# Kernel optimization log

Hardware: AMD Instinct MI355X
Metric: run time of the kernel (lower is better)

The kernel has to match this reference:

```python
import jax, jax.numpy as jnp
import numpy as np

B, N, S = 32, 4096, 11          # batch, n_inputs (64x64 feature map), n_slots
D_IN, D, MLP = 512, 512, 2048   # input feat dim, qkv_size, mlp hidden
ITERS = 3                       # num_iterations
EPS_ATTN = 1e-8                 # renormalize epsilon
EPS_LN = 1e-5                   # torch LayerNorm default eps


def layer_norm(x, g, b, eps=EPS_LN):
    mu = jnp.mean(x, axis=-1, keepdims=True)
    var = jnp.mean(jnp.square(x - mu), axis=-1, keepdims=True)
    return (x - mu) * jax.lax.rsqrt(var + eps) * g + b


def setup_inputs() -> dict:
    key = jax.random.key(0)
    ks = jax.random.split(key, 16)
    s = 0.02
    return {
        "slots": jax.random.normal(ks[0], (B, S, D), jnp.float32),
        "inputs": jax.random.normal(ks[1], (B, N, D_IN), jnp.float32),
        # input LayerNorm
        "ln_in_g": jnp.ones((D_IN,), jnp.float32),
        "ln_in_b": jnp.zeros((D_IN,), jnp.float32),
        # k / v projections (with bias, like nn.Linear)
        "Wk": jax.random.normal(ks[2], (D_IN, D), jnp.float32) * s,
        "bk": jnp.zeros((D,), jnp.float32),
        "Wv": jax.random.normal(ks[3], (D_IN, D), jnp.float32) * s,
        "bv": jnp.zeros((D,), jnp.float32),
        # query LayerNorm + bias-free q projection
        "ln_q_g": jnp.ones((D,), jnp.float32),
        "ln_q_b": jnp.zeros((D,), jnp.float32),
        "Wq": jax.random.normal(ks[4], (D, D), jnp.float32) * s,
        # GRUCell: gate order (r, z, n), torch layout [3D, D]
        "W_ih": jax.random.normal(ks[5], (3 * D, D), jnp.float32) * s,
        "b_ih": jnp.zeros((3 * D,), jnp.float32),
        "W_hh": jax.random.normal(ks[6], (3 * D, D), jnp.float32) * s,
        "b_hh": jnp.zeros((3 * D,), jnp.float32),
        # MLP: LN -> Linear -> ReLU -> Linear (no residual in source)
        "ln_m_g": jnp.ones((D,), jnp.float32),
        "ln_m_b": jnp.zeros((D,), jnp.float32),
        "W1": jax.random.normal(ks[7], (D, MLP), jnp.float32) * s,
        "b1": jnp.zeros((MLP,), jnp.float32),
        "W2": jax.random.normal(ks[8], (MLP, D), jnp.float32) * s,
        "b2": jnp.zeros((D,), jnp.float32),
    }


def reference(slots, inputs, ln_in_g, ln_in_b, Wk, bk, Wv, bv,
              ln_q_g, ln_q_b, Wq, W_ih, b_ih, W_hh, b_hh,
              ln_m_g, ln_m_b, W1, b1, W2, b2):
    # inputs LN + k/v projections (computed once, outside the loop)
    x = layer_norm(inputs, ln_in_g, ln_in_b)          # [B, N, D_IN]
    k = x @ Wk + bk                                   # [B, N, D]
    v = x @ Wv + bv                                   # [B, N, D]
    scale = 1.0 / jnp.sqrt(jnp.asarray(D, slots.dtype))

    for _ in range(ITERS):
        # q projection
        q = layer_norm(slots, ln_q_g, ln_q_b) @ Wq    # [B, S, D]
        # inverted attention: softmax over slot (query) axis
        logits = jnp.einsum('bsd,bnd->bsn', q * scale, k)  # [B, S, N]
        attn = jax.nn.softmax(logits, axis=-2)        # over S (inverted)
        # renormalize over keys (mean norm)
        attn = attn / (jnp.sum(attn, axis=-1, keepdims=True) + EPS_ATTN)
        updates = jnp.einsum('bsn,bnd->bsd', attn, v)  # [B, S, D]

        # GRUCell(updates, slots) -- torch semantics, gate order (r, z, n)
        gi = updates @ W_ih.T + b_ih                  # [B, S, 3D]
        gh = slots @ W_hh.T + b_hh                    # [B, S, 3D]
        ir, iz, in_ = jnp.split(gi, 3, axis=-1)
        hr, hz, hn = jnp.split(gh, 3, axis=-1)
        r = jax.nn.sigmoid(ir + hr)
        z = jax.nn.sigmoid(iz + hz)
        n = jnp.tanh(in_ + r * hn)
        slots = (1.0 - z) * n + z * slots

        # MLP (note: source assigns slots = mlp(slots), no residual)
        h = layer_norm(slots, ln_m_g, ln_m_b)
        slots = jax.nn.relu(h @ W1 + b1) @ W2 + b2
    return slots
```

## Files before the change

kernel.cpp:

```cpp
#include <hip/hip_runtime.h>
#include <cstdint>
#include <cstddef>

typedef short bf16x8 __attribute__((ext_vector_type(8)));
typedef float floatx4 __attribute__((ext_vector_type(4)));
typedef unsigned short ushort4v __attribute__((ext_vector_type(4)));

#define LN_EPS 1e-5f
#define ATTN_EPS 1e-8f
#define NCHUNK 16

__device__ __forceinline__ unsigned short f2bf(float f) {
    unsigned int u = __float_as_uint(f);
    u += 0x7fffu + ((u >> 16) & 1u);
    return (unsigned short)(u >> 16);
}

__device__ __forceinline__ void load_lds16(const void* gp, void* lp) {
    __builtin_amdgcn_global_load_lds(
        (__attribute__((address_space(1))) void*)gp,
        (__attribute__((address_space(3))) void*)lp,
        16, 0, 0);
}

template<bool OUT_BF16, bool QDOT>
__global__ __launch_bounds__(256) void ln512_kernel(
        const float* __restrict__ x, const float* __restrict__ g, const float* __restrict__ b,
        void* __restrict__ out, int total_rows, int data_rows, float outscale,
        const float* __restrict__ wqbk, float* __restrict__ cbuf) {
    int row = blockIdx.x * 4 + (threadIdx.x >> 6);
    int lane = threadIdx.x & 63;
    if (row >= total_rows) return;
    int rr = row < data_rows ? row : data_rows - 1;
    const float4* xr = (const float4*)(x + (size_t)rr * 512);
    float4 a0 = xr[lane];
    float4 a1 = xr[lane + 64];
    float s  = a0.x + a0.y + a0.z + a0.w + a1.x + a1.y + a1.z + a1.w;
    float ss = a0.x*a0.x + a0.y*a0.y + a0.z*a0.z + a0.w*a0.w
             + a1.x*a1.x + a1.y*a1.y + a1.z*a1.z + a1.w*a1.w;
    #pragma unroll
    for (int off = 32; off > 0; off >>= 1) {
        s  += __shfl_xor(s, off, 64);
        ss += __shfl_xor(ss, off, 64);
    }
    float mu = s * (1.0f / 512.0f);
    float var = ss * (1.0f / 512.0f) - mu * mu;
    float rstd = rsqrtf(var + LN_EPS);
    float4 g0 = ((const float4*)g)[lane];
    float4 g1 = ((const float4*)g)[lane + 64];
    float4 b0 = ((const float4*)b)[lane];
    float4 b1 = ((const float4*)b)[lane + 64];
    float y[8];
    y[0] = ((a0.x - mu) * rstd * g0.x + b0.x) * outscale;
    y[1] = ((a0.y - mu) * rstd * g0.y + b0.y) * outscale;
    y[2] = ((a0.z - mu) * rstd * g0.z + b0.z) * outscale;
    y[3] = ((a0.w - mu) * rstd * g0.w + b0.w) * outscale;
    y[4] = ((a1.x - mu) * rstd * g1.x + b1.x) * outscale;
    y[5] = ((a1.y - mu) * rstd * g1.y + b1.y) * outscale;
    y[6] = ((a1.z - mu) * rstd * g1.z + b1.z) * outscale;
    y[7] = ((a1.w - mu) * rstd * g1.w + b1.w) * outscale;
    if (QDOT) {
        float4 w0 = ((const float4*)wqbk)[lane];
        float4 w1 = ((const float4*)wqbk)[lane + 64];
        float cd = y[0]*w0.x + y[1]*w0.y + y[2]*w0.z + y[3]*w0.w
                 + y[4]*w1.x + y[5]*w1.y + y[6]*w1.z + y[7]*w1.w;
        #pragma unroll
        for (int off = 32; off > 0; off >>= 1) cd += __shfl_xor(cd, off, 64);
        if (lane == 0) cbuf[row] = cd;
    }
    if (OUT_BF16) {
        unsigned short* orow = (unsigned short*)out + (size_t)row * 512;
        ushort4v o0, o1;
        o0.x = f2bf(y[0]); o0.y = f2bf(y[1]); o0.z = f2bf(y[2]); o0.w = f2bf(y[3]);
        o1.x = f2bf(y[4]); o1.y = f2bf(y[5]); o1.z = f2bf(y[6]); o1.w = f2bf(y[7]);
        *(ushort4v*)(orow + lane * 4) = o0;
        *(ushort4v*)(orow + 256 + lane * 4) = o1;
    } else {
        float* orow = (float*)out + (size_t)row * 512;
        *(float4*)(orow + lane * 4) = make_float4(y[0], y[1], y[2], y[3]);
        *(float4*)(orow + 256 + lane * 4) = make_float4(y[4], y[5], y[6], y[7]);
    }
}

__device__ __forceinline__ void tr32(const float* __restrict__ in, unsigned short* __restrict__ out,
                                     int R, int C, int bx, int by, float (*tile)[33]) {
    int tx = threadIdx.x & 31, ty = threadIdx.x >> 5;
    #pragma unroll
    for (int i = 0; i < 32; i += 8)
        tile[ty + i][tx] = in[(size_t)(by + ty + i) * C + bx + tx];
    __syncthreads();
    #pragma unroll
    for (int i = 0; i < 32; i += 8)
        out[(size_t)(bx + ty + i) * R + by + tx] = f2bf(tile[tx][ty + i]);
}

__device__ __forceinline__ void rowdot512(const float* __restrict__ in, const float* __restrict__ vec,
                                          float* __restrict__ out, int row) {
    int lane = threadIdx.x & 63;
    const float4* r0 = (const float4*)(in + (size_t)row * 512);
    float4 a0 = r0[lane], a1 = r0[lane + 64];
    float4 v0 = ((const float4*)vec)[lane], v1 = ((const float4*)vec)[lane + 64];
    float d = a0.x*v0.x + a0.y*v0.y + a0.z*v0.z + a0.w*v0.w
            + a1.x*v1.x + a1.y*v1.y + a1.z*v1.z + a1.w*v1.w;
    #pragma unroll
    for (int off = 32; off > 0; off >>= 1) d += __shfl_xor(d, off, 64);
    if (lane == 0) out[row] = d;
}

__global__ __launch_bounds__(256) void prep_all(
        const float* __restrict__ Wk, const float* __restrict__ Wq,
        const float* __restrict__ Wv, const float* __restrict__ W_ih,
        const float* __restrict__ W_hh, const float* __restrict__ W1,
        const float* __restrict__ W2, const float* __restrict__ slots_in,
        const float* __restrict__ bk, const float* __restrict__ bv,
        unsigned short* __restrict__ Wk_b, unsigned short* __restrict__ Wq_b,
        unsigned short* __restrict__ Wv_b, unsigned short* __restrict__ Wih_b,
        unsigned short* __restrict__ Whh_b, unsigned short* __restrict__ W1T,
        unsigned short* __restrict__ W2T, unsigned short* __restrict__ slbf,
        float* __restrict__ wqbk, float* __restrict__ bvW) {
    __shared__ float tile[32][33];
    const int b = blockIdx.x;
    const int t = threadIdx.x;
    if (b < 1024) {
        int idx = b * 256 + t; Wk_b[idx] = f2bf(Wk[idx]);
    } else if (b < 2048) {
        int idx = (b - 1024) * 256 + t; Wq_b[idx] = f2bf(Wq[idx]);
    } else if (b < 3072) {
        int idx = (b - 2048) * 256 + t; Wv_b[idx] = f2bf(Wv[idx]);
    } else if (b < 6144) {
        int idx = (b - 3072) * 256 + t; Wih_b[idx] = f2bf(W_ih[idx]);
    } else if (b < 9216) {
        int idx = (b - 6144) * 256 + t; Whh_b[idx] = f2bf(W_hh[idx]);
    } else if (b < 10240) {
        int i = b - 9216;
        tr32(W1, W1T, 512, 2048, (i & 63) * 32, (i >> 6) * 32, tile);
    } else if (b < 11264) {
        int i = b - 10240;
        tr32(W2, W2T, 2048, 512, (i & 15) * 32, (i >> 4) * 32, tile);
    } else if (b < 12032) {
        int idx = (b - 11264) * 256 + t;
        int row = idx >> 9, d = idx & 511;
        int rr = row < 352 ? row : 351;
        slbf[idx] = f2bf(slots_in[(size_t)rr * 512 + d]);
    } else if (b < 12160) {
        int row = (b - 12032) * 4 + (t >> 6);
        rowdot512(Wq, bk, wqbk, row);
    } else {
        int row = (b - 12160) * 4 + (t >> 6);
        rowdot512(W_ih, bv, bvW, row);
    }
}

template<int BMODE, bool RELU, int OUT_MODE>
__device__ __forceinline__ void hgemm_core(
        const unsigned short* __restrict__ A, const unsigned short* __restrict__ Bt,
        const float* __restrict__ bias, const float* __restrict__ bvW,
        const float* __restrict__ coef, float* __restrict__ Cf,
        unsigned short* __restrict__ Cb, int m0, int n0, int N, int K,
        unsigned short* As, unsigned short* Bs) {
    const int t = threadIdx.x;
    const int lane = t & 63;
    const int w = t >> 6;
    const int wm = w >> 1, wn = w & 1;
    const int quad = lane >> 4;
    const int l15 = lane & 15;
    floatx4 acc[2][2];
    #pragma unroll
    for (int i = 0; i < 2; ++i)
        #pragma unroll
        for (int j = 0; j < 2; ++j)
            #pragma unroll
            for (int r = 0; r < 4; ++r) acc[i][j][r] = 0.0f;

    for (int k0 = 0; k0 < K; k0 += 64) {
        #pragma unroll
        for (int p = 0; p < 2; ++p) {
            const int s = p * 256 + t;
            const int row = s >> 3;
            const int c = (s & 7) ^ (row & 7);
            const int ldsoff = (s - lane) * 16;
            load_lds16(A  + (size_t)(m0 + row) * K + k0 + c * 8, (char*)As + ldsoff);
            load_lds16(Bt + (size_t)(n0 + row) * K + k0 + c * 8, (char*)Bs + ldsoff);
        }
        __builtin_amdgcn_s_waitcnt(0);
        __syncthreads();
        #pragma unroll
        for (int h = 0; h < 2; ++h) {
            bf16x8 af[2], bfr[2];
            #pragma unroll
            for (int i = 0; i < 2; ++i) {
                const int row = wm * 32 + i * 16 + l15;
                const int cp = ((h << 2) | quad) ^ (l15 & 7);
                af[i] = *(const bf16x8*)(As + row * 64 + cp * 8);
            }
            #pragma unroll
            for (int j = 0; j < 2; ++j) {
                const int row = wn * 32 + j * 16 + l15;
                const int cp = ((h << 2) | quad) ^ (l15 & 7);
                bfr[j] = *(const bf16x8*)(Bs + row * 64 + cp * 8);
            }
            #pragma unroll
            for (int i = 0; i < 2; ++i)
                #pragma unroll
                for (int j = 0; j < 2; ++j)
                    acc[i][j] = __builtin_amdgcn_mfma_f32_16x16x32_bf16(af[i], bfr[j], acc[i][j], 0, 0, 0);
        }
        __syncthreads();
    }
    #pragma unroll
    for (int j = 0; j < 2; ++j) {
        const int n = n0 + wn * 32 + j * 16 + l15;
        const float bb = (BMODE >= 1) ? bias[n] : 0.0f;
        const float bw = (BMODE == 2) ? bvW[n] : 0.0f;
        #pragma unroll
        for (int i = 0; i < 2; ++i) {
            #pragma unroll
            for (int r = 0; r < 4; ++r) {
                const int m = m0 + wm * 32 + i * 16 + quad * 4 + r;
                float v = acc[i][j][r] + bb;
                if (BMODE == 2) v += coef[m] * bw;
                if (RELU) v = fmaxf(v, 0.0f);
                if (OUT_MODE == 0 || OUT_MODE == 2) Cf[(size_t)m * N + n] = v;
                if (OUT_MODE == 1 || OUT_MODE == 2) Cb[(size_t)m * N + n] = f2bf(v);
            }
        }
    }
}

template<int BMODE, bool RELU, int OUT_MODE>
__global__ __launch_bounds__(256) void hgemm(
        const unsigned short* __restrict__ A, const unsigned short* __restrict__ Bt,
        const float* __restrict__ bias, float* __restrict__ Cf,
        unsigned short* __restrict__ Cb, int N, int K) {
    __shared__ unsigned short As[64 * 64];
    __shared__ unsigned short Bs[64 * 64];
    hgemm_core<BMODE, RELU, OUT_MODE>(A, Bt, bias, nullptr, nullptr, Cf, Cb,
                                      blockIdx.y * 64, blockIdx.x * 64, N, K, As, Bs);
}

__global__ __launch_bounds__(256) void prep_gemms(
        const unsigned short* __restrict__ Wk_b, const unsigned short* __restrict__ Wq_b,
        const unsigned short* __restrict__ Wih_b, const unsigned short* __restrict__ Wv_b,
        unsigned short* __restrict__ WqkT, unsigned short* __restrict__ Wc) {
    __shared__ unsigned short As[64 * 64];
    __shared__ unsigned short Bs[64 * 64];
    if (blockIdx.z == 0) {
        if (blockIdx.y >= 8) return;
        hgemm_core<0, false, 1>(Wk_b, Wq_b, nullptr, nullptr, nullptr, nullptr, WqkT,
                                blockIdx.y * 64, blockIdx.x * 64, 512, 512, As, Bs);
    } else {
        hgemm_core<0, false, 1>(Wih_b, Wv_b, nullptr, nullptr, nullptr, nullptr, Wc,
                                blockIdx.y * 64, blockIdx.x * 64, 512, 512, As, Bs);
    }
}

__global__ __launch_bounds__(256) void gru_gemm(
        const unsigned short* __restrict__ Pn, const unsigned short* __restrict__ slbf,
        const unsigned short* __restrict__ Wc, const unsigned short* __restrict__ Whh,
        const float* __restrict__ bih, const float* __restrict__ bhh,
        const float* __restrict__ bvW, const float* __restrict__ coef,
        float* __restrict__ gi, float* __restrict__ gh) {
    __shared__ unsigned short As[64 * 64];
    __shared__ unsigned short Bs[64 * 64];
    if (blockIdx.z == 0)
        hgemm_core<2, false, 0>(Pn, Wc, bih, bvW, coef, gi, nullptr,
                                blockIdx.y * 64, blockIdx.x * 64, 1536, 512, As, Bs);
    else
        hgemm_core<1, false, 0>(slbf, Whh, bhh, nullptr, nullptr, gh, nullptr,
                                blockIdx.y * 64, blockIdx.x * 64, 1536, 512, As, Bs);
}

__global__ __launch_bounds__(256, 2) void attn_kernel(
        const unsigned short* __restrict__ qp_b, const unsigned short* __restrict__ xln,
        const float* __restrict__ cbuf,
        float* __restrict__ Up, float* __restrict__ rsp) {
    const int b = blockIdx.y;
    const int chunk = blockIdx.x;
    const int w = threadIdx.x >> 6, lane = threadIdx.x & 63;
    const int l15 = lane & 15, quad = lane >> 4;
    const int d0 = lane * 8;
    const int NPC = 4096 / NCHUNK;

    __shared__ float attnlds[4][16][20];
    __shared__ float Us[11 * 512];
    __shared__ float rss[11];

    const unsigned short* qrow = qp_b + (size_t)(b * 11 + (l15 < 11 ? l15 : 10)) * 512 + quad * 8;
    bf16x8 aq[16];
    #pragma unroll
    for (int ks = 0; ks < 16; ++ks) aq[ks] = *(const bf16x8*)(qrow + ks * 32);

    float cb[4];
    #pragma unroll
    for (int r = 0; r < 4; ++r) {
        int s = quad * 4 + r;
        cb[r] = (s < 11) ? cbuf[b * 11 + s] : 0.0f;
    }

    float U[11][8];
    float rs[11];
    #pragma unroll
    for (int s = 0; s < 11; ++s) {
        rs[s] = 0.f;
        #pragma unroll
        for (int j = 0; j < 8; ++j) U[s][j] = 0.f;
    }

    const unsigned short* xbase = xln + ((size_t)b * 4096 + (size_t)chunk * NPC) * 512;

    for (int t = 0; t < NPC / 64; ++t) {
        const int n0 = t * 64 + w * 16;
        const unsigned short* krow = xbase + (size_t)(n0 + l15) * 512 + quad * 8;
        floatx4 c;
        c[0] = c[1] = c[2] = c[3] = 0.0f;
        #pragma unroll
        for (int ks = 0; ks < 16; ++ks) {
            bf16x8 bf = *(const bf16x8*)(krow + ks * 32);
            c = __builtin_amdgcn_mfma_f32_16x16x32_bf16(aq[ks], bf, c, 0, 0, 0);
        }
        float l0 = c[0] + cb[0], l1 = c[1] + cb[1], l2 = c[2] + cb[2], l3 = c[3] + cb[3];
        if (quad == 2) l3 = -1e30f;
        if (quad == 3) { l0 = -1e30f; l1 = -1e30f; l2 = -1e30f; l3 = -1e30f; }
        float mx = fmaxf(fmaxf(l0, l1), fmaxf(l2, l3));
        mx = fmaxf(mx, __shfl_xor(mx, 16, 64));
        mx = fmaxf(mx, __shfl_xor(mx, 32, 64));
        float e0 = __expf(l0 - mx), e1 = __expf(l1 - mx),
              e2 = __expf(l2 - mx), e3 = __expf(l3 - mx);
        float se = e0 + e1 + e2 + e3;
        se += __shfl_xor(se, 16, 64);
        se += __shfl_xor(se, 32, 64);
        float inv = 1.0f / se;
        float4 av = make_float4(e0 * inv, e1 * inv, e2 * inv, e3 * inv);
        *(float4*)&attnlds[w][l15][quad * 4] = av;
        __builtin_amdgcn_wave_barrier();
        for (int nl = 0; nl < 16; ++nl) {
            uint4 kr = *(const uint4*)(xbase + (size_t)(n0 + nl) * 512 + d0);
            float kf[8];
            kf[0] = __uint_as_float(kr.x << 16); kf[1] = __uint_as_float(kr.x & 0xffff0000u);
            kf[2] = __uint_as_float(kr.y << 16); kf[3] = __uint_as_float(kr.y & 0xffff0000u);
            kf[4] = __uint_as_float(kr.z << 16); kf[5] = __uint_as_float(kr.z & 0xffff0000u);
            kf[6] = __uint_as_float(kr.w << 16); kf[7] = __uint_as_float(kr.w & 0xffff0000u);
            float4 a0 = *(const float4*)&attnlds[w][nl][0];
            float4 a1 = *(const float4*)&attnlds[w][nl][4];
            float4 a2 = *(const float4*)&attnlds[w][nl][8];
            float as[11] = {a0.x, a0.y, a0.z, a0.w, a1.x, a1.y, a1.z, a1.w,
                            a2.x, a2.y, a2.z};
            #pragma unroll
            for (int s = 0; s < 11; ++s) {
                rs[s] += as[s];
                #pragma unroll
                for (int j = 0; j < 8; ++j) U[s][j] = fmaf(as[s], kf[j], U[s][j]);
            }
        }
    }

    for (int ph = 0; ph < 4; ++ph) {
        if (w == ph) {
            #pragma unroll
            for (int s = 0; s < 11; ++s) {
                #pragma unroll
                for (int j = 0; j < 8; ++j) {
                    if (ph == 0) Us[s * 512 + d0 + j] = U[s][j];
                    else         Us[s * 512 + d0 + j] += U[s][j];
                }
            }
            if (lane == 0) {
                #pragma unroll
                for (int s = 0; s < 11; ++s) {
                    if (ph == 0) rss[s] = rs[s]; else rss[s] += rs[s];
                }
            }
        }
        __syncthreads();
    }
    float* up = Up + ((size_t)b * NCHUNK + chunk) * 11 * 512;
    for (int idx = threadIdx.x; idx < 11 * 512; idx += 256) up[idx] = Us[idx];
    if (threadIdx.x < 11) rsp[((size_t)b * NCHUNK + chunk) * 11 + threadIdx.x] = rss[threadIdx.x];
}

__global__ __launch_bounds__(256) void attn_reduce(
        const float* __restrict__ Up, const float* __restrict__ rsp,
        unsigned short* __restrict__ Pn, float* __restrict__ coef) {
    const int bs = blockIdx.x;
    if (bs >= 352) {
        for (int d = threadIdx.x; d < 512; d += 256) Pn[(size_t)bs * 512 + d] = 0;
        if (threadIdx.x == 0) coef[bs] = 0.0f;
        return;
    }
    const int b = bs / 11, s = bs - b * 11;
    float rsum = 0.0f;
    #pragma unroll
    for (int c = 0; c < NCHUNK; ++c) rsum += rsp[((size_t)b * NCHUNK + c) * 11 + s];
    const float inv = 1.0f / (rsum + ATTN_EPS);
    if (threadIdx.x == 0) coef[bs] = rsum * inv;
    for (int d = threadIdx.x; d < 512; d += 256) {
        float acc = 0.f;
        #pragma unroll
        for (int c = 0; c < NCHUNK; ++c) acc += Up[(((size_t)b * NCHUNK + c) * 11 + s) * 512 + d];
        Pn[(size_t)bs * 512 + d] = f2bf(acc * inv);
    }
}

__global__ __launch_bounds__(256) void gru_ln(
        const float* __restrict__ gi, const float* __restrict__ gh,
        const float* __restrict__ slots, const float* __restrict__ g,
        const float* __restrict__ b, unsigned short* __restrict__ mln) {
    int row = blockIdx.x * 4 + (threadIdx.x >> 6);
    int lane = threadIdx.x & 63;
    unsigned short* orow = mln + (size_t)row * 512;
    if (row >= 352) {
        ushort4v z; z.x = z.y = z.z = z.w = 0;
        *(ushort4v*)(orow + lane * 4) = z;
        *(ushort4v*)(orow + 256 + lane * 4) = z;
        return;
    }
    const float4* gir = (const float4*)(gi + (size_t)row * 1536);
    const float4* ghr = (const float4*)(gh + (size_t)row * 1536);
    const float4* sr  = (const float4*)(slots + (size_t)row * 512);
    float v[8];
    #pragma unroll
    for (int half = 0; half < 2; ++half) {
        int o = half * 64 + lane;
        float4 ir = gir[o], iz = gir[128 + o], in_ = gir[256 + o];
        float4 hr = ghr[o], hz = ghr[128 + o], hn = ghr[256 + o];
        float4 sv = sr[o];
        float rr[4], zz[4], nn[4];
        rr[0] = 1.f / (1.f + __expf(-(ir.x + hr.x)));
        rr[1] = 1.f / (1.f + __expf(-(ir.y + hr.y)));
        rr[2] = 1.f / (1.f + __expf(-(ir.z + hr.z)));
        rr[3] = 1.f / (1.f + __expf(-(ir.w + hr.w)));
        zz[0] = 1.f / (1.f + __expf(-(iz.x + hz.x)));
        zz[1] = 1.f / (1.f + __expf(-(iz.y + hz.y)));
        zz[2] = 1.f / (1.f + __expf(-(iz.z + hz.z)));
        zz[3] = 1.f / (1.f + __expf(-(iz.w + hz.w)));
        nn[0] = tanhf(in_.x + rr[0] * hn.x);
        nn[1] = tanhf(in_.y + rr[1] * hn.y);
        nn[2] = tanhf(in_.z + rr[2] * hn.z);
        nn[3] = tanhf(in_.w + rr[3] * hn.w);
        v[half * 4 + 0] = (1.f - zz[0]) * nn[0] + zz[0] * sv.x;
        v[half * 4 + 1] = (1.f - zz[1]) * nn[1] + zz[1] * sv.y;
        v[half * 4 + 2] = (1.f - zz[2]) * nn[2] + zz[2] * sv.z;
        v[half * 4 + 3] = (1.f - zz[3]) * nn[3] + zz[3] * sv.w;
    }
    float s = 0.f, ss = 0.f;
    #pragma unroll
    for (int j = 0; j < 8; ++j) { s += v[j]; ss += v[j] * v[j]; }
    #pragma unroll
    for (int off = 32; off > 0; off >>= 1) {
        s  += __shfl_xor(s, off, 64);
        ss += __shfl_xor(ss, off, 64);
    }
    float mu = s * (1.0f / 512.0f);
    float var = ss * (1.0f / 512.0f) - mu * mu;
    float rstd = rsqrtf(var + LN_EPS);
    float4 g0 = ((const float4*)g)[lane], g1 = ((const float4*)g)[lane + 64];
    float4 b0 = ((const float4*)b)[lane], b1 = ((const float4*)b)[lane + 64];
    ushort4v o0, o1;
    o0.x = f2bf((v[0] - mu) * rstd * g0.x + b0.x);
    o0.y = f2bf((v[1] - mu) * rstd * g0.y + b0.y);
    o0.z = f2bf((v[2] - mu) * rstd * g0.z + b0.z);
    o0.w = f2bf((v[3] - mu) * rstd * g0.w + b0.w);
    o1.x = f2bf((v[4] - mu) * rstd * g1.x + b1.x);
    o1.y = f2bf((v[5] - mu) * rstd * g1.y + b1.y);
    o1.z = f2bf((v[6] - mu) * rstd * g1.z + b1.z);
    o1.w = f2bf((v[7] - mu) * rstd * g1.w + b1.w);
    *(ushort4v*)(orow + lane * 4) = o0;
    *(ushort4v*)(orow + 256 + lane * 4) = o1;
}

extern "C" void kernel_launch(void* const* d_in, const int* in_sizes, int n_in,
                              void* d_out, int out_size, void* d_ws, size_t ws_size,
                              hipStream_t stream) {
    const float* slots_in = (const float*)d_in[0];
    const float* inputs   = (const float*)d_in[1];
    const float* ln_in_g  = (const float*)d_in[2];
    const float* ln_in_b  = (const float*)d_in[3];
    const float* Wk  = (const float*)d_in[4];
    const float* bk  = (const float*)d_in[5];
    const float* Wv  = (const float*)d_in[6];
    const float* bv  = (const float*)d_in[7];
    const float* ln_q_g = (const float*)d_in[8];
    const float* ln_q_b = (const float*)d_in[9];
    const float* Wq  = (const float*)d_in[10];
    const float* W_ih = (const float*)d_in[11];
    const float* b_ih = (const float*)d_in[12];
    const float* W_hh = (const float*)d_in[13];
    const float* b_hh = (const float*)d_in[14];
    const float* ln_m_g = (const float*)d_in[15];
    const float* ln_m_b = (const float*)d_in[16];
    const float* W1 = (const float*)d_in[17];
    const float* b1 = (const float*)d_in[18];
    const float* W2 = (const float*)d_in[19];
    const float* b2 = (const float*)d_in[20];

    char* p = (char*)d_ws;
    auto alloc = [&](size_t bytes) { char* r = p; p += (bytes + 255) & ~(size_t)255; return r; };
    unsigned short* xln   = (unsigned short*)alloc(131072ull * 512 * 2);
    unsigned short* Wk_b  = (unsigned short*)alloc(512ull * 512 * 2);
    unsigned short* Wq_b  = (unsigned short*)alloc(512ull * 512 * 2);
    unsigned short* Wv_b  = (unsigned short*)alloc(512ull * 512 * 2);
    unsigned short* Wih_b = (unsigned short*)alloc(1536ull * 512 * 2);
    unsigned short* Whh_b = (unsigned short*)alloc(1536ull * 512 * 2);
    unsigned short* WqkT  = (unsigned short*)alloc(512ull * 512 * 2);
    unsigned short* Wc    = (unsigned short*)alloc(1536ull * 512 * 2);
    unsigned short* W1T   = (unsigned short*)alloc(2048ull * 512 * 2);
    unsigned short* W2T   = (unsigned short*)alloc(512ull * 2048 * 2);
    unsigned short* slq   = (unsigned short*)alloc(384ull * 512 * 2);
    unsigned short* mln   = (unsigned short*)alloc(384ull * 512 * 2);
    unsigned short* Pn    = (unsigned short*)alloc(384ull * 512 * 2);
    unsigned short* slbf  = (unsigned short*)alloc(384ull * 512 * 2);
    unsigned short* h1    = (unsigned short*)alloc(384ull * 2048 * 2);
    unsigned short* qp_b  = (unsigned short*)alloc(384ull * 512 * 2);
    float* slots = (float*)alloc(384ull * 512 * 4);
    float* gi    = (float*)alloc(384ull * 1536 * 4);
    float* gh    = (float*)alloc(384ull * 1536 * 4);
    float* Up    = (float*)alloc((size_t)32 * NCHUNK * 11 * 512 * 4);
    float* rsp   = (float*)alloc((size_t)32 * NCHUNK * 11 * 4);
    float* wqbk  = (float*)alloc(512 * 4);
    float* bvW   = (float*)alloc(1536 * 4);
    float* cbuf  = (float*)alloc(384 * 4);
    float* coef  = (float*)alloc(384 * 4);

    ln512_kernel<true, false><<<dim3(32768), 256, 0, stream>>>(
        inputs, ln_in_g, ln_in_b, xln, 131072, 131072, 1.0f, nullptr, nullptr);
    prep_all<<<dim3(12544), 256, 0, stream>>>(
        Wk, Wq, Wv, W_ih, W_hh, W1, W2, slots_in, bk, bv,
        Wk_b, Wq_b, Wv_b, Wih_b, Whh_b, W1T, W2T, slbf, wqbk, bvW);
    prep_gemms<<<dim3(8, 24, 2), 256, 0, stream>>>(Wk_b, Wq_b, Wih_b, Wv_b, WqkT, Wc);
    hipMemcpyAsync(slots, slots_in, 352ull * 512 * 4, hipMemcpyDeviceToDevice, stream);

    const float qscale = 0.044194173824159216f;
    for (int it = 0; it < 3; ++it) {
        ln512_kernel<true, true><<<dim3(96), 256, 0, stream>>>(
            slots, ln_q_g, ln_q_b, slq, 384, 352, qscale, wqbk, cbuf);
        hgemm<0, false, 1><<<dim3(8, 6), 256, 0, stream>>>(slq, WqkT, nullptr, nullptr, qp_b, 512, 512);
        attn_kernel<<<dim3(NCHUNK, 32), 256, 0, stream>>>(qp_b, xln, cbuf, Up, rsp);
        attn_reduce<<<dim3(384), 256, 0, stream>>>(Up, rsp, Pn, coef);
        gru_gemm<<<dim3(24, 6, 2), 256, 0, stream>>>(Pn, slbf, Wc, Whh_b, b_ih, b_hh, bvW, coef, gi, gh);
        gru_ln<<<dim3(96), 256, 0, stream>>>(gi, gh, slots, ln_m_g, ln_m_b, mln);
        hgemm<1, true, 1><<<dim3(32, 6), 256, 0, stream>>>(mln, W1T, b1, nullptr, h1, 2048, 512);
        hgemm<1, false, 2><<<dim3(8, 6), 256, 0, stream>>>(h1, W2T, b2, slots, slbf, 512, 2048);
    }
    hipMemcpyAsync(d_out, slots, (size_t)out_size * 4, hipMemcpyDeviceToDevice, stream);
}
```

Baseline: 745.2 us.

## Fuse iteration loop into a persistent cooperative kernel with grid syncs

After: 1.565 ms. +110.0%, slower.

```diff
diff --git a/kernel.cpp b/kernel.cpp
--- a/kernel.cpp
+++ b/kernel.cpp
@@ -1,6 +1,9 @@
 #include <hip/hip_runtime.h>
+#include <hip/hip_cooperative_groups.h>
 #include <cstdint>
 #include <cstddef>
+
+namespace cg = cooperative_groups;
 
 typedef short bf16x8 __attribute__((ext_vector_type(8)));
 typedef float floatx4 __attribute__((ext_vector_type(4)));
@@ -24,11 +27,11 @@
 }
 
 template<bool OUT_BF16, bool QDOT>
-__global__ __launch_bounds__(256) void ln512_kernel(
+__device__ __forceinline__ void ln512_body(
         const float* __restrict__ x, const float* __restrict__ g, const float* __restrict__ b,
         void* __restrict__ out, int total_rows, int data_rows, float outscale,
-        const float* __restrict__ wqbk, float* __restrict__ cbuf) {
-    int row = blockIdx.x * 4 + (threadIdx.x >> 6);
+        const float* __restrict__ wqbk, float* __restrict__ cbuf, int blk) {
+    int row = blk * 4 + (threadIdx.x >> 6);
     int lane = threadIdx.x & 63;
     if (row >= total_rows) return;
     int rr = row < data_rows ? row : data_rows - 1;
@@ -82,6 +85,14 @@
     }
 }
 
+template<bool OUT_BF16, bool QDOT>
+__global__ __launch_bounds__(256) void ln512_kernel(
+        const float* __restrict__ x, const float* __restrict__ g, const float* __restrict__ b,
+        void* __restrict__ out, int total_rows, int data_rows, float outscale,
+        const float* __restrict__ wqbk, float* __restrict__ cbuf) {
+    ln512_body<OUT_BF16, QDOT>(x, g, b, out, total_rows, data_rows, outscale, wqbk, cbuf, blockIdx.x);
+}
+
 __device__ __forceinline__ void tr32(const float* __restrict__ in, unsigned short* __restrict__ out,
                                      int R, int C, int bx, int by, float (*tile)[33]) {
     int tx = threadIdx.x & 31, ty = threadIdx.x >> 5;
@@ -117,7 +128,7 @@
         unsigned short* __restrict__ Wv_b, unsigned short* __restrict__ Wih_b,
         unsigned short* __restrict__ Whh_b, unsigned short* __restrict__ W1T,
         unsigned short* __restrict__ W2T, unsigned short* __restrict__ slbf,
-        float* __restrict__ wqbk, float* __restrict__ bvW) {
+        float* __restrict__ wqbk, float* __restrict__ bvW, float* __restrict__ slots) {
     __shared__ float tile[32][33];
     const int b = blockIdx.x;
     const int t = threadIdx.x;
@@ -145,9 +156,12 @@
     } else if (b < 12160) {
         int row = (b - 12032) * 4 + (t >> 6);
         rowdot512(Wq, bk, wqbk, row);
-    } else {
+    } else if (b < 12288) {
         int row = (b - 12160) * 4 + (t >> 6);
         rowdot512(W_ih, bv, bvW, row);
+    } else {
+        int idx = (b - 12288) * 256 + t;
+        slots[idx] = slots_in[idx];
     }
 }
 
@@ -270,20 +284,16 @@
                                 blockIdx.y * 64, blockIdx.x * 64, 1536, 512, As, Bs);
 }
 
-__global__ __launch_bounds__(256, 2) void attn_kernel(
+__device__ __forceinline__ void attn_body(
+        int b, int chunk,
         const unsigned short* __restrict__ qp_b, const unsigned short* __restrict__ xln,
         const float* __restrict__ cbuf,
-        float* __restrict__ Up, float* __restrict__ rsp) {
-    const int b = blockIdx.y;
-    const int chunk = blockIdx.x;
+        float* __restrict__ Up, float* __restrict__ rsp,
+        float* __restrict__ Us, float* __restrict__ attnlds, float* __restrict__ rss) {
     const int w = threadIdx.x >> 6, lane = threadIdx.x & 63;
     const int l15 = lane & 15, quad = lane >> 4;
     const int d0 = lane * 8;
     const int NPC = 4096 / NCHUNK;
-
-    __shared__ float attnlds[4][16][20];
-    __shared__ float Us[11 * 512];
-    __shared__ float rss[11];
 
     const unsigned short* qrow = qp_b + (size_t)(b * 11 + (l15 < 11 ? l15 : 10)) * 512 + quad * 8;
     bf16x8 aq[16];
@@ -331,7 +341,7 @@
         se += __shfl_xor(se, 32, 64);
         float inv = 1.0f / se;
         float4 av = make_float4(e0 * inv, e1 * inv, e2 * inv, e3 * inv);
-        *(float4*)&attnlds[w][l15][quad * 4] = av;
+        *(float4*)&attnlds[(w * 16 + l15) * 20 + quad * 4] = av;
         __builtin_amdgcn_wave_barrier();
         for (int nl = 0; nl < 16; ++nl) {
             uint4 kr = *(const uint4*)(xbase + (size_t)(n0 + nl) * 512 + d0);
@@ -340,9 +350,10 @@
             kf[2] = __uint_as_float(kr.y << 16); kf[3] = __uint_as_float(kr.y & 0xffff0000u);
             kf[4] = __uint_as_float(kr.z << 16); kf[5] = __uint_as_float(kr.z & 0xffff0000u);
             kf[6] = __uint_as_float(kr.w << 16); kf[7] = __uint_as_float(kr.w & 0xffff0000u);
-            float4 a0 = *(const float4*)&attnlds[w][nl][0];
-            float4 a1 = *(const float4*)&attnlds[w][nl][4];
-            float4 a2 = *(const float4*)&attnlds[w][nl][8];
+            const float* arow = &attnlds[(w * 16 + nl) * 20];
+            float4 a0 = *(const float4*)(arow);
+            float4 a1 = *(const float4*)(arow + 4);
+            float4 a2 = *(const float4*)(arow + 8);
             float as[11] = {a0.x, a0.y, a0.z, a0.w, a1.x, a1.y, a1.z, a1.w,
                             a2.x, a2.y, a2.z};
             #pragma unroll
@@ -376,12 +387,22 @@
     float* up = Up + ((size_t)b * NCHUNK + chunk) * 11 * 512;
     for (int idx = threadIdx.x; idx < 11 * 512; idx += 256) up[idx] = Us[idx];
     if (threadIdx.x < 11) rsp[((size_t)b * NCHUNK + chunk) * 11 + threadIdx.x] = rss[threadIdx.x];
-}
-
-__global__ __launch_bounds__(256) void attn_reduce(
-        const float* __restrict__ Up, const float* __restrict__ rsp,
+    __syncthreads();
+}
+
+__global__ __launch_bounds__(256, 2) void attn_kernel(
+        const unsigned short* __restrict__ qp_b, const unsigned short* __restrict__ xln,
+        const float* __restrict__ cbuf,
+        float* __restrict__ Up, float* __restrict__ rsp) {
+    __shared__ float Us[11 * 512];
+    __shared__ float attnlds[64 * 20];
+    __shared__ float rss[11];
+    attn_body(blockIdx.y, blockIdx.x, qp_b, xln, cbuf, Up, rsp, Us, attnlds, rss);
+}
+
+__device__ __forceinline__ void attn_reduce_body(
+        int bs, const float* __restrict__ Up, const float* __restrict__ rsp,
         unsigned short* __restrict__ Pn, float* __restrict__ coef) {
-    const int bs = blockIdx.x;
     if (bs >= 352) {
         for (int d = threadIdx.x; d < 512; d += 256) Pn[(size_t)bs * 512 + d] = 0;
         if (threadIdx.x == 0) coef[bs] = 0.0f;
@@ -401,11 +422,17 @@
     }
 }
 
-__global__ __launch_bounds__(256) void gru_ln(
+__global__ __launch_bounds__(256) void attn_reduce(
+        const float* __restrict__ Up, const float* __restrict__ rsp,
+        unsigned short* __restrict__ Pn, float* __restrict__ coef) {
+    attn_reduce_body(blockIdx.x, Up, rsp, Pn, coef);
+}
+
+__device__ __forceinline__ void gru_ln_body(
         const float* __restrict__ gi, const float* __restrict__ gh,
         const float* __restrict__ slots, const float* __restrict__ g,
-        const float* __restrict__ b, unsigned short* __restrict__ mln) {
-    int row = blockIdx.x * 4 + (threadIdx.x >> 6);
+        const float* __restrict__ b, unsigned short* __restrict__ mln, int blk) {
+    int row = blk * 4 + (threadIdx.x >> 6);
     int lane = threadIdx.x & 63;
     unsigned short* orow = mln + (size_t)row * 512;
     if (row >= 352) {
@@ -466,6 +493,85 @@
     o1.w = f2bf((v[7] - mu) * rstd * g1.w + b1.w);
     *(ushort4v*)(orow + lane * 4) = o0;
     *(ushort4v*)(orow + 256 + lane * 4) = o1;
+}
+
+__global__ __launch_bounds__(256) void gru_ln(
+        const float* __restrict__ gi, const float* __restrict__ gh,
+        const float* __restrict__ slots, const float* __restrict__ g,
+        const float* __restrict__ b, unsigned short* __restrict__ mln) {
+    gru_ln_body(gi, gh, slots, g, b, mln, blockIdx.x);
+}
+
+struct IterArgs {
+    float* slots;
+    const float* ln_q_g; const float* ln_q_b;
+    unsigned short* slq;
+    const unsigned short* WqkT;
+    unsigned short* qp_b;
+    const unsigned short* xln;
+    float* cbuf;
+    float* Up; float* rsp;
+    unsigned short* Pn; float* coef;
+    const unsigned short* Wc; const unsigned short* Whh;
+    const float* b_ih; const float* b_hh; const float* bvW;
+    float* gi; float* gh;
+    const float* ln_m_g; const float* ln_m_b;
+    unsigned short* mln;
+    const unsigned short* W1T; const float* b1; unsigned short* h1;
+    const unsigned short* W2T; const float* b2; unsigned short* slbf;
+    const float* wqbk;
+};
+
+__global__ __launch_bounds__(256, 2) void iter_kernel(IterArgs a) {
+    cg::grid_group grid = cg::this_grid();
+    const int G = gridDim.x;
+    const int bid = blockIdx.x;
+    __shared__ unsigned short As[64 * 64];
+    __shared__ unsigned short Bs[64 * 64];
+    __shared__ float Us[11 * 512];
+    __shared__ float attnlds[64 * 20];
+    __shared__ float rss[11];
+    const float qscale = 0.044194173824159216f;
+
+    for (int it = 0; it < 3; ++it) {
+        for (int j = bid; j < 96; j += G)
+            ln512_body<true, true>(a.slots, a.ln_q_g, a.ln_q_b, a.slq, 384, 352, qscale,
+                                   a.wqbk, a.cbuf, j);
+        grid.sync();
+        for (int j = bid; j < 48; j += G)
+            hgemm_core<0, false, 1>(a.slq, a.WqkT, nullptr, nullptr, nullptr, nullptr, a.qp_b,
+                                    (j >> 3) * 64, (j & 7) * 64, 512, 512, As, Bs);
+        grid.sync();
+        for (int j = bid; j < 32 * NCHUNK; j += G)
+            attn_body(j >> 4, j & (NCHUNK - 1), a.qp_b, a.xln, a.cbuf, a.Up, a.rsp,
+                      Us, attnlds, rss);
+        grid.sync();
+        for (int j = bid; j < 384; j += G)
+            attn_reduce_body(j, a.Up, a.rsp, a.Pn, a.coef);
+        grid.sync();
+        for (int j = bid; j < 288; j += G) {
+            int z = j / 144, r = j - z * 144;
+            int x = r % 24, y = r / 24;
+            if (z == 0)
+                hgemm_core<2, false, 0>(a.Pn, a.Wc, a.b_ih, a.bvW, a.coef, a.gi, nullptr,
+                                        y * 64, x * 64, 1536, 512, As, Bs);
+            else
+                hgemm_core<1, false, 0>(a.slbf, a.Whh, a.b_hh, nullptr, nullptr, a.gh, nullptr,
+                                        y * 64, x * 64, 1536, 512, As, Bs);
+        }
+        grid.sync();
+        for (int j = bid; j < 96; j += G)
+            gru_ln_body(a.gi, a.gh, a.slots, a.ln_m_g, a.ln_m_b, a.mln, j);
+        grid.sync();
+        for (int j = bid; j < 192; j += G)
+            hgemm_core<1, true, 1>(a.mln, a.W1T, a.b1, nullptr, nullptr, nullptr, a.h1,
+                                   (j >> 5) * 64, (j & 31) * 64, 2048, 512, As, Bs);
+        grid.sync();
+        for (int j = bid; j < 48; j += G)
+            hgemm_core<1, false, 2>(a.h1, a.W2T, a.b2, nullptr, nullptr, a.slots, a.slbf,
+                                    (j >> 3) * 64, (j & 7) * 64, 512, 2048, As, Bs);
+        grid.sync();
+    }
 }
 
 extern "C" void kernel_launch(void* const* d_in, const int* in_sizes, int n_in,
@@ -523,23 +629,42 @@
 
     ln512_kernel<true, false><<<dim3(32768), 256, 0, stream>>>(
         inputs, ln_in_g, ln_in_b, xln, 131072, 131072, 1.0f, nullptr, nullptr);
-    prep_all<<<dim3(12544), 256, 0, stream>>>(
+    prep_all<<<dim3(12992), 256, 0, stream>>>(
         Wk, Wq, Wv, W_ih, W_hh, W1, W2, slots_in, bk, bv,
-        Wk_b, Wq_b, Wv_b, Wih_b, Whh_b, W1T, W2T, slbf, wqbk, bvW);
+        Wk_b, Wq_b, Wv_b, Wih_b, Whh_b, W1T, W2T, slbf, wqbk, bvW, slots);
     prep_gemms<<<dim3(8, 24, 2), 256, 0, stream>>>(Wk_b, Wq_b, Wih_b, Wv_b, WqkT, Wc);
-    hipMemcpyAsync(slots, slots_in, 352ull * 512 * 4, hipMemcpyDeviceToDevice, stream);
-
-    const float qscale = 0.044194173824159216f;
-    for (int it = 0; it < 3; ++it) {
-        ln512_kernel<true, true><<<dim3(96), 256, 0, stream>>>(
-            slots, ln_q_g, ln_q_b, slq, 384, 352, qscale, wqbk, cbuf);
-        hgemm<0, false, 1><<<dim3(8, 6), 256, 0, stream>>>(slq, WqkT, nullptr, nullptr, qp_b, 512, 512);
-        attn_kernel<<<dim3(NCHUNK, 32), 256, 0, stream>>>(qp_b, xln, cbuf, Up, rsp);
-        attn_reduce<<<dim3(384), 256, 0, stream>>>(Up, rsp, Pn, coef);
-        gru_gemm<<<dim3(24, 6, 2), 256, 0, stream>>>(Pn, slbf, Wc, Whh_b, b_ih, b_hh, bvW, coef, gi, gh);
-        gru_ln<<<dim3(96), 256, 0, stream>>>(gi, gh, slots, ln_m_g, ln_m_b, mln);
-        hgemm<1, true, 1><<<dim3(32, 6), 256, 0, stream>>>(mln, W1T, b1, nullptr, h1, 2048, 512);
-        hgemm<1, false, 2><<<dim3(8, 6), 256, 0, stream>>>(h1, W2T, b2, slots, slbf, 512, 2048);
+
+    IterArgs ia;
+    ia.slots = slots; ia.ln_q_g = ln_q_g; ia.ln_q_b = ln_q_b; ia.slq = slq;
+    ia.WqkT = WqkT; ia.qp_b = qp_b; ia.xln = xln; ia.cbuf = cbuf;
+    ia.Up = Up; ia.rsp = rsp; ia.Pn = Pn; ia.coef = coef;
+    ia.Wc = Wc; ia.Whh = Whh_b; ia.b_ih = b_ih; ia.b_hh = b_hh; ia.bvW = bvW;
+    ia.gi = gi; ia.gh = gh; ia.ln_m_g = ln_m_g; ia.ln_m_b = ln_m_b; ia.mln = mln;
+    ia.W1T = W1T; ia.b1 = b1; ia.h1 = h1; ia.W2T = W2T; ia.b2 = b2; ia.slbf = slbf;
+    ia.wqbk = wqbk;
+
+    int maxb = 0;
+    if (hipOccupancyMaxActiveBlocksPerMultiprocessor(&maxb, iter_kernel, 256, 0) != hipSuccess
+        || maxb < 1) maxb = 1;
+    int nblk = maxb >= 2 ? 512 : 256;
+
+    void* kargs[] = {(void*)&ia};
+    hipError_t cerr = hipLaunchCooperativeKernel((const void*)iter_kernel,
+                                                 dim3(nblk), dim3(256), kargs, 0, stream);
+    if (cerr != hipSuccess) {
+        (void)hipGetLastError();
+        const float qscale = 0.044194173824159216f;
+        for (int it = 0; it < 3; ++it) {
+            ln512_kernel<true, true><<<dim3(96), 256, 0, stream>>>(
+                slots, ln_q_g, ln_q_b, slq, 384, 352, qscale, wqbk, cbuf);
+            hgemm<0, false, 1><<<dim3(8, 6), 256, 0, stream>>>(slq, WqkT, nullptr, nullptr, qp_b, 512, 512);
+            attn_kernel<<<dim3(NCHUNK, 32), 256, 0, stream>>>(qp_b, xln, cbuf, Up, rsp);
+            attn_reduce<<<dim3(384), 256, 0, stream>>>(Up, rsp, Pn, coef);
+            gru_gemm<<<dim3(24, 6, 2), 256, 0, stream>>>(Pn, slbf, Wc, Whh_b, b_ih, b_hh, bvW, coef, gi, gh);
+            gru_ln<<<dim3(96), 256, 0, stream>>>(gi, gh, slots, ln_m_g, ln_m_b, mln);
+            hgemm<1, true, 1><<<dim3(32, 6), 256, 0, stream>>>(mln, W1T, b1, nullptr, h1, 2048, 512);
+            hgemm<1, false, 2><<<dim3(8, 6), 256, 0, stream>>>(h1, W2T, b2, slots, slbf, 512, 2048);
+        }
     }
     hipMemcpyAsync(d_out, slots, (size_t)out_size * 4, hipMemcpyDeviceToDevice, stream);
 }
```
